# Optimization experiments

Hardware: AMD Instinct MI355X
Metric: run time of the kernel (lower is better)

Reference implementation:

```python
import jax, jax.numpy as jnp
import numpy as np

N_EXPERTS = 8
D_IN = 512
D_OUT = 512


def setup_inputs() -> dict:
    key = jax.random.key(0)
    k1, k2, k3, k4 = jax.random.split(key, 4)
    B, N = 16, 4096
    z = jax.random.randint(k1, (B, N), 0, N_EXPERTS, dtype=jnp.int64 if jax.config.jax_enable_x64 else jnp.int32)
    x = jax.random.normal(k2, (B, N, D_IN), dtype=jnp.float32)
    # Expert parameters: map_list[e] modeled as Linear(D_IN, D_OUT)
    W = jax.random.normal(k3, (N_EXPERTS, D_IN, D_OUT), dtype=jnp.float32) * (1.0 / np.sqrt(D_IN))
    b = jax.random.normal(k4, (N_EXPERTS, D_OUT), dtype=jnp.float32) * 0.01
    return {"z": z, "x": x, "W": W, "b": b}


def reference(z, x, W, b):
    B, N = z.shape
    z_flat = z.reshape(-1)                 # [T]
    x_flat = x.reshape(-1, x.shape[-1])    # [T, D_in]
    T = z_flat.shape[0]
    y = jnp.zeros((T, D_OUT), dtype=x.dtype)
    # Dense equivalent of mask-gather -> expert apply -> masked scatter.
    # Tokens with id == -1 (or any id not hit) stay zero, matching the torch code.
    for e in range(N_EXPERTS):
        mask = (z_flat == e)[:, None]      # [T, 1]
        y_e = x_flat @ W[e] + b[e]         # [T, D_out]
        y = jnp.where(mask, y_e, y)
    y = y.reshape(B, N, D_OUT)
    return (z, y)
```

## Files before the change

kernel.cpp:

```cpp
#include <hip/hip_runtime.h>
#include <stdint.h>

#define NEXP 8
#define DD   512
#define BM   128
#define BN   128

typedef short s16x8 __attribute__((ext_vector_type(8)));
typedef float f32x4 __attribute__((ext_vector_type(4)));

static __device__ __forceinline__ unsigned short f2bf(float f) {
    union { float f; unsigned u; } v; v.f = f;
    unsigned r = v.u + 0x7FFFu + ((v.u >> 16) & 1u);
    return (unsigned short)(r >> 16);
}


__global__ void hist_kernel(const int* __restrict__ z, int* __restrict__ counts, int T) {
    __shared__ int lc[NEXP];
    int tid = threadIdx.x;
    if (tid < NEXP) lc[tid] = 0;
    __syncthreads();
    int t = blockIdx.x * blockDim.x + tid;
    if (t < T) atomicAdd(&lc[z[t]], 1);
    __syncthreads();
    if (tid < NEXP) atomicAdd(&counts[tid], lc[tid]);
}

__global__ void scan_kernel(const int* __restrict__ counts, int* __restrict__ cursors,
                            int4* __restrict__ table, int max_tiles) {
    __shared__ int off[NEXP + 1];
    __shared__ int tb[NEXP + 1];
    int tid = threadIdx.x;
    if (tid == 0) {
        int o = 0, tbs = 0;
        for (int e = 0; e < NEXP; e++) {
            off[e] = o; tb[e] = tbs;
            cursors[e] = o;
            int c = counts[e];
            o += c;
            tbs += (c + BM - 1) / BM;
        }
        off[NEXP] = o; tb[NEXP] = tbs;
    }
    __syncthreads();
    for (int idx = tid; idx < max_tiles; idx += blockDim.x) {
        int4 ent; ent.x = -1; ent.y = 0; ent.z = 0; ent.w = 0;
#pragma unroll
        for (int e = 0; e < NEXP; e++) {
            if (idx >= tb[e] && idx < tb[e + 1]) {
                int r = (idx - tb[e]) * BM;
                ent.x = e; ent.y = off[e] + r; ent.z = (off[e + 1] - off[e]) - r;
            }
        }
        table[idx] = ent;
    }
}

__global__ void scatter_kernel(const int* __restrict__ z, int* __restrict__ cursors,
                               int* __restrict__ token_index, float* __restrict__ zout, int T) {
    __shared__ int lc[NEXP];
    __shared__ int lbase[NEXP];
    int tid = threadIdx.x;
    if (tid < NEXP) lc[tid] = 0;
    __syncthreads();
    int t = blockIdx.x * blockDim.x + tid;
    int e = 0, rank = 0;
    if (t < T) {
        e = z[t];
        rank = atomicAdd(&lc[e], 1);
        zout[t] = (float)e;
    }
    __syncthreads();
    if (tid < NEXP) lbase[tid] = atomicAdd(&cursors[tid], lc[tid]);
    __syncthreads();
    if (t < T) token_index[lbase[e] + rank] = t;
}

__global__ __launch_bounds__(256) void gather_kernel(const float* __restrict__ x,
                                                     const int* __restrict__ token_index,
                                                     unsigned short* __restrict__ xg, int T) {
    int i = blockIdx.x * 4 + (threadIdx.x >> 6);
    if (i >= T) return;
    int lane = threadIdx.x & 63;
    int t = token_index[i];
    const float4* src = (const float4*)(x + (size_t)t * DD) + lane * 2;
    float4 v0 = src[0], v1 = src[1];
    uint4 p;
    p.x = (unsigned)f2bf(v0.x) | ((unsigned)f2bf(v0.y) << 16);
    p.y = (unsigned)f2bf(v0.z) | ((unsigned)f2bf(v0.w) << 16);
    p.z = (unsigned)f2bf(v1.x) | ((unsigned)f2bf(v1.y) << 16);
    p.w = (unsigned)f2bf(v1.z) | ((unsigned)f2bf(v1.w) << 16);
    *(uint4*)(xg + (size_t)i * DD + lane * 8) = p;
}

__global__ void convw_kernel(const float* __restrict__ W, unsigned short* __restrict__ Wt) {
    __shared__ float tile[32][33];
    int e = blockIdx.z, k0 = blockIdx.x * 32, n0 = blockIdx.y * 32;
    int tid = threadIdx.x;
    const float* We = W + (size_t)e * DD * DD;
    unsigned short* WtE = Wt + (size_t)e * DD * DD;
    int c = tid & 31, r0 = tid >> 5;
#pragma unroll
    for (int i = 0; i < 4; i++) {
        int kr = r0 + 8 * i;
        tile[kr][c] = We[(size_t)(k0 + kr) * DD + n0 + c];
    }
    __syncthreads();
#pragma unroll
    for (int i = 0; i < 4; i++) {
        int nr = r0 + 8 * i;
        WtE[(size_t)(n0 + nr) * DD + k0 + c] = f2bf(tile[c][nr]);
    }
}


__global__ __launch_bounds__(256) void gemm2_kernel(
    const unsigned short* __restrict__ xg,
    const unsigned short* __restrict__ Wt,
    const float* __restrict__ bias,
    const int* __restrict__ token_index,
    const int4* __restrict__ table,
    float* __restrict__ y)
{
    int4 te = table[blockIdx.x];
    int e = te.x;
    if (e < 0) return;
    const int base = te.y;
    const int rows_valid = te.z < BM ? te.z : BM;
    const int n0 = blockIdx.y * BN;

    __shared__ unsigned short Als[BM * 64];
    __shared__ unsigned short Bls[BN * 64];

    const int tid  = threadIdx.x;
    const int lane = tid & 63;
    const int wave = tid >> 6;
    const int wm = (wave & 1) * 64;
    const int wn = (wave >> 1) * 64;

    int srow[4], schunk[4];
#pragma unroll
    for (int q = 0; q < 4; q++) {
        int s = wave * 256 + q * 64 + lane;
        srow[q]   = s >> 3;
        schunk[q] = (s & 7) ^ ((s >> 3) & 7);
    }

    const unsigned short* WtE = Wt + (size_t)e * DD * DD;

    f32x4 acc[4][4];
#pragma unroll
    for (int i = 0; i < 4; i++)
#pragma unroll
        for (int j = 0; j < 4; j++) acc[i][j] = (f32x4){0.f, 0.f, 0.f, 0.f};

    const int quad = lane >> 4;
    const int lrow = lane & 15;

    for (int k0 = 0; k0 < DD; k0 += 64) {
        __syncthreads();
#pragma unroll
        for (int q = 0; q < 4; q++) {
            const int r = srow[q], c = schunk[q];
            const unsigned short* ga = xg + (size_t)(base + r) * DD + k0 + c * 8;
            const unsigned short* gb = WtE + (size_t)(n0 + r) * DD + k0 + c * 8;
            unsigned short* la = &Als[(size_t)(wave * 256 + q * 64) * 8];
            unsigned short* lb = &Bls[(size_t)(wave * 256 + q * 64) * 8];
            __builtin_amdgcn_global_load_lds((const __attribute__((address_space(1))) void*)ga,
                                             (__attribute__((address_space(3))) void*)la, 16, 0, 0);
            __builtin_amdgcn_global_load_lds((const __attribute__((address_space(1))) void*)gb,
                                             (__attribute__((address_space(3))) void*)lb, 16, 0, 0);
        }
        __syncthreads();

#pragma unroll
        for (int ks = 0; ks < 2; ks++) {
            s16x8 af[4], bq[4];
#pragma unroll
            for (int i = 0; i < 4; i++) {
                int r = wm + i * 16 + lrow;
                af[i] = *(const s16x8*)(&Als[r * 64 + (((quad + 4 * ks) ^ (r & 7)) * 8)]);
            }
#pragma unroll
            for (int j = 0; j < 4; j++) {
                int r = wn + j * 16 + lrow;
                bq[j] = *(const s16x8*)(&Bls[r * 64 + (((quad + 4 * ks) ^ (r & 7)) * 8)]);
            }
#pragma unroll
            for (int i = 0; i < 4; i++)
#pragma unroll
                for (int j = 0; j < 4; j++)
                    acc[i][j] = __builtin_amdgcn_mfma_f32_16x16x32_bf16(af[i], bq[j], acc[i][j], 0, 0, 0);
        }
    }

    const int lcol = lane & 15;
    float bv[4];
#pragma unroll
    for (int j = 0; j < 4; j++) bv[j] = bias[e * DD + n0 + wn + j * 16 + lcol];
#pragma unroll
    for (int i = 0; i < 4; i++) {
#pragma unroll
        for (int reg = 0; reg < 4; reg++) {
            int r = wm + i * 16 + quad * 4 + reg;
            if (r < rows_valid) {
                int t = token_index[base + r];
                float* yr = y + (size_t)t * DD + n0 + wn + lcol;
#pragma unroll
                for (int j = 0; j < 4; j++)
                    yr[j * 16] = acc[i][j][reg] + bv[j];
            }
        }
    }
}


__global__ __launch_bounds__(256) void gemm_kernel(
    const float* __restrict__ x, const unsigned short* __restrict__ Wt,
    const float* __restrict__ bias, const int* __restrict__ token_index,
    const int4* __restrict__ table, float* __restrict__ y)
{
    int4 te = table[blockIdx.x];
    int e = te.x;
    if (e < 0) return;
    int base = te.y;
    int rows_valid = te.z < BM ? te.z : BM;
    int n0 = blockIdx.y * BN;

    __shared__ unsigned short Als[BM * 40];
    __shared__ unsigned short Bls[BN * 40];

    const int tid  = threadIdx.x;
    const int lane = tid & 63;
    const int wave = tid >> 6;
    const int wm = (wave & 1) * 64;
    const int wn = (wave >> 1) * 64;

    const int a_q  = tid & 7;
    const int a_r0 = tid >> 3;
    int tok[4];
#pragma unroll
    for (int i = 0; i < 4; i++) {
        int r = a_r0 + 32 * i;
        int rr = (r < rows_valid) ? r : 0;
        tok[i] = token_index[base + rr];
    }
    const int b_c  = tid & 3;
    const int b_n0 = tid >> 2;
    const unsigned short* WtE = Wt + (size_t)e * DD * DD;

    f32x4 acc[4][4];
#pragma unroll
    for (int i = 0; i < 4; i++)
#pragma unroll
        for (int j = 0; j < 4; j++) acc[i][j] = (f32x4){0.f, 0.f, 0.f, 0.f};

    const int quad = lane >> 4;
    const int lrow = lane & 15;

    for (int k0 = 0; k0 < DD; k0 += 32) {
        __syncthreads();
#pragma unroll
        for (int i = 0; i < 4; i++) {
            int r = a_r0 + 32 * i;
            const float4 v = *(const float4*)(x + (size_t)tok[i] * DD + k0 + a_q * 4);
            unsigned u0 = (unsigned)f2bf(v.x) | ((unsigned)f2bf(v.y) << 16);
            unsigned u1 = (unsigned)f2bf(v.z) | ((unsigned)f2bf(v.w) << 16);
            uint2 p; p.x = u0; p.y = u1;
            *(uint2*)(&Als[r * 40 + a_q * 4]) = p;
        }
#pragma unroll
        for (int i = 0; i < 2; i++) {
            int n = b_n0 + 64 * i;
            uint4 v = *(const uint4*)(WtE + (size_t)(n0 + n) * DD + k0 + b_c * 8);
            *(uint4*)(&Bls[n * 40 + b_c * 8]) = v;
        }
        __syncthreads();

        s16x8 af[4], bq[4];
#pragma unroll
        for (int i = 0; i < 4; i++)
            af[i] = *(const s16x8*)(&Als[(wm + i * 16 + lrow) * 40 + quad * 8]);
#pragma unroll
        for (int j = 0; j < 4; j++)
            bq[j] = *(const s16x8*)(&Bls[(wn + j * 16 + lrow) * 40 + quad * 8]);
#pragma unroll
        for (int i = 0; i < 4; i++)
#pragma unroll
            for (int j = 0; j < 4; j++)
                acc[i][j] = __builtin_amdgcn_mfma_f32_16x16x32_bf16(af[i], bq[j], acc[i][j], 0, 0, 0);
    }

    const int lcol = lane & 15;
    float bv[4];
#pragma unroll
    for (int j = 0; j < 4; j++) bv[j] = bias[e * DD + n0 + wn + j * 16 + lcol];
#pragma unroll
    for (int i = 0; i < 4; i++) {
#pragma unroll
        for (int reg = 0; reg < 4; reg++) {
            int r = wm + i * 16 + quad * 4 + reg;
            if (r < rows_valid) {
                int t = token_index[base + r];
                float* yr = y + (size_t)t * DD + n0 + wn + lcol;
#pragma unroll
                for (int j = 0; j < 4; j++)
                    yr[j * 16] = acc[i][j][reg] + bv[j];
            }
        }
    }
}


extern "C" void kernel_launch(void* const* d_in, const int* in_sizes, int n_in,
                              void* d_out, int out_size, void* d_ws, size_t ws_size,
                              hipStream_t stream) {
    const int*   z = (const int*)d_in[0];
    const float* x = (const float*)d_in[1];
    const float* W = (const float*)d_in[2];
    const float* b = (const float*)d_in[3];
    const int T = in_sizes[0];

    float* zout = (float*)d_out;
    float* y    = (float*)d_out + T;

    char* ws = (char*)d_ws;
    int*  counts      = (int*)ws;
    int*  cursors     = (int*)(ws + 64);
    int4* table       = (int4*)(ws + 256);
    int*  token_index = (int*)(ws + 16640);
    unsigned short* Wt = (unsigned short*)(ws + 278784);
    unsigned short* xg = (unsigned short*)(ws + 4473344);

    const int max_tiles = T / BM + NEXP;
    const size_t need = 4473344 + (size_t)T * DD * 2 + 131072;

    hipMemsetAsync(ws, 0, 64, stream);
    hist_kernel<<<(T + 255) / 256, 256, 0, stream>>>(z, counts, T);
    convw_kernel<<<dim3(DD / 32, DD / 32, NEXP), 256, 0, stream>>>(W, Wt);
    scan_kernel<<<1, 256, 0, stream>>>(counts, cursors, table, max_tiles);
    scatter_kernel<<<(T + 255) / 256, 256, 0, stream>>>(z, cursors, token_index, zout, T);

    if (ws_size >= need) {
        gather_kernel<<<(T + 3) / 4, 256, 0, stream>>>(x, token_index, xg, T);
        gemm2_kernel<<<dim3(max_tiles, DD / BN), 256, 0, stream>>>(xg, Wt, b, token_index, table, y);
    } else {
        gemm_kernel<<<dim3(max_tiles, DD / BN), 256, 0, stream>>>(x, Wt, b, token_index, table, y);
    }
}
```

Before: 333.7 us.

## Fuse prep kernels, merge scatter with gather, remap GEMM grid for XCD locality

Merges weight conversion and the expert histogram into one launch, and fuses the token scatter with the x gather/bf16 conversion so x is read in token order and written to its sorted slot. The GEMM grid is flattened and remapped so the four N-subtiles of the same row tile land on the same XCD, which should improve L2 reuse of the activation tile. This cuts launch count and one pass over token_index, but now uses scattered writes in the gather and needs max_tiles to be a multiple of 8 for the remap to cover every tile.

```diff
diff --git a/kernel.cpp b/kernel.cpp
--- a/kernel.cpp
+++ b/kernel.cpp
@@ -15,16 +15,38 @@
     return (unsigned short)(r >> 16);
 }
 
-
-__global__ void hist_kernel(const int* __restrict__ z, int* __restrict__ counts, int T) {
+__global__ __launch_bounds__(256) void prep_kernel(const float* __restrict__ W,
+                                                   unsigned short* __restrict__ Wt,
+                                                   const int* __restrict__ z,
+                                                   int* __restrict__ counts, int T) {
+    __shared__ float tile[32][33];
     __shared__ int lc[NEXP];
+    int bid = blockIdx.x;
     int tid = threadIdx.x;
-    if (tid < NEXP) lc[tid] = 0;
-    __syncthreads();
-    int t = blockIdx.x * blockDim.x + tid;
-    if (t < T) atomicAdd(&lc[z[t]], 1);
-    __syncthreads();
-    if (tid < NEXP) atomicAdd(&counts[tid], lc[tid]);
+    if (bid < 2048) {
+        int e = bid >> 8, k0 = ((bid >> 4) & 15) * 32, n0 = (bid & 15) * 32;
+        const float* We = W + (size_t)e * DD * DD;
+        unsigned short* WtE = Wt + (size_t)e * DD * DD;
+        int c = tid & 31, r0 = tid >> 5;
+#pragma unroll
+        for (int i = 0; i < 4; i++) {
+            int kr = r0 + 8 * i;
+            tile[kr][c] = We[(size_t)(k0 + kr) * DD + n0 + c];
+        }
+        __syncthreads();
+#pragma unroll
+        for (int i = 0; i < 4; i++) {
+            int nr = r0 + 8 * i;
+            WtE[(size_t)(n0 + nr) * DD + k0 + c] = f2bf(tile[c][nr]);
+        }
+    } else {
+        if (tid < NEXP) lc[tid] = 0;
+        __syncthreads();
+        int t = (bid - 2048) * 256 + tid;
+        if (t < T) atomicAdd(&lc[z[t]], 1);
+        __syncthreads();
+        if (tid < NEXP) atomicAdd(&counts[tid], lc[tid]);
+    }
 }
 
 __global__ void scan_kernel(const int* __restrict__ counts, int* __restrict__ cursors,
@@ -57,63 +79,51 @@
     }
 }
 
-__global__ void scatter_kernel(const int* __restrict__ z, int* __restrict__ cursors,
-                               int* __restrict__ token_index, float* __restrict__ zout, int T) {
+__global__ __launch_bounds__(256) void scatgat_kernel(
+    const int* __restrict__ z, const float* __restrict__ x,
+    int* __restrict__ cursors, int* __restrict__ token_index,
+    float* __restrict__ zout, unsigned short* __restrict__ xg, int T)
+{
     __shared__ int lc[NEXP];
     __shared__ int lbase[NEXP];
-    int tid = threadIdx.x;
+    __shared__ int ldst[64];
+    int tid = threadIdx.x, wave = tid >> 6, lane = tid & 63;
+    int t0 = blockIdx.x * 64;
     if (tid < NEXP) lc[tid] = 0;
     __syncthreads();
-    int t = blockIdx.x * blockDim.x + tid;
+    int t = t0 + wave * 16 + lane;
     int e = 0, rank = 0;
-    if (t < T) {
+    bool own = (lane < 16) && (t < T);
+    if (own) {
         e = z[t];
         rank = atomicAdd(&lc[e], 1);
         zout[t] = (float)e;
     }
     __syncthreads();
-    if (tid < NEXP) lbase[tid] = atomicAdd(&cursors[tid], lc[tid]);
-    __syncthreads();
-    if (t < T) token_index[lbase[e] + rank] = t;
-}
-
-__global__ __launch_bounds__(256) void gather_kernel(const float* __restrict__ x,
-                                                     const int* __restrict__ token_index,
-                                                     unsigned short* __restrict__ xg, int T) {
-    int i = blockIdx.x * 4 + (threadIdx.x >> 6);
-    if (i >= T) return;
-    int lane = threadIdx.x & 63;
-    int t = token_index[i];
-    const float4* src = (const float4*)(x + (size_t)t * DD) + lane * 2;
-    float4 v0 = src[0], v1 = src[1];
-    uint4 p;
-    p.x = (unsigned)f2bf(v0.x) | ((unsigned)f2bf(v0.y) << 16);
-    p.y = (unsigned)f2bf(v0.z) | ((unsigned)f2bf(v0.w) << 16);
-    p.z = (unsigned)f2bf(v1.x) | ((unsigned)f2bf(v1.y) << 16);
-    p.w = (unsigned)f2bf(v1.z) | ((unsigned)f2bf(v1.w) << 16);
-    *(uint4*)(xg + (size_t)i * DD + lane * 8) = p;
-}
-
-__global__ void convw_kernel(const float* __restrict__ W, unsigned short* __restrict__ Wt) {
-    __shared__ float tile[32][33];
-    int e = blockIdx.z, k0 = blockIdx.x * 32, n0 = blockIdx.y * 32;
-    int tid = threadIdx.x;
-    const float* We = W + (size_t)e * DD * DD;
-    unsigned short* WtE = Wt + (size_t)e * DD * DD;
-    int c = tid & 31, r0 = tid >> 5;
-#pragma unroll
-    for (int i = 0; i < 4; i++) {
-        int kr = r0 + 8 * i;
-        tile[kr][c] = We[(size_t)(k0 + kr) * DD + n0 + c];
-    }
-    __syncthreads();
-#pragma unroll
-    for (int i = 0; i < 4; i++) {
-        int nr = r0 + 8 * i;
-        WtE[(size_t)(n0 + nr) * DD + k0 + c] = f2bf(tile[c][nr]);
-    }
-}
-
+    if (tid < NEXP) lbase[tid] = lc[tid] ? atomicAdd(&cursors[tid], lc[tid]) : 0;
+    __syncthreads();
+    if (own) {
+        int dst = lbase[e] + rank;
+        token_index[dst] = t;
+        ldst[wave * 16 + lane] = dst;
+    }
+    __syncthreads();
+#pragma unroll
+    for (int rr = 0; rr < 16; rr++) {
+        int idx = wave * 16 + rr;
+        int src_t = t0 + idx;
+        if (src_t >= T) break;
+        int dst = ldst[idx];
+        const float4* src = (const float4*)(x + (size_t)src_t * DD) + lane * 2;
+        float4 v0 = src[0], v1 = src[1];
+        uint4 p;
+        p.x = (unsigned)f2bf(v0.x) | ((unsigned)f2bf(v0.y) << 16);
+        p.y = (unsigned)f2bf(v0.z) | ((unsigned)f2bf(v0.w) << 16);
+        p.z = (unsigned)f2bf(v1.x) | ((unsigned)f2bf(v1.y) << 16);
+        p.w = (unsigned)f2bf(v1.z) | ((unsigned)f2bf(v1.w) << 16);
+        *(uint4*)(xg + (size_t)dst * DD + lane * 8) = p;
+    }
+}
 
 __global__ __launch_bounds__(256) void gemm2_kernel(
     const unsigned short* __restrict__ xg,
@@ -123,12 +133,16 @@
     const int4* __restrict__ table,
     float* __restrict__ y)
 {
-    int4 te = table[blockIdx.x];
+    const int bid    = blockIdx.x;
+    const int xcd    = bid & 7;
+    const int nsub   = (bid >> 3) & 3;
+    const int tileid = ((bid >> 5) << 3) | xcd;
+    int4 te = table[tileid];
     int e = te.x;
     if (e < 0) return;
     const int base = te.y;
     const int rows_valid = te.z < BM ? te.z : BM;
-    const int n0 = blockIdx.y * BN;
+    const int n0 = nsub * BN;
 
     __shared__ unsigned short Als[BM * 64];
     __shared__ unsigned short Bls[BN * 64];
@@ -215,6 +229,26 @@
     }
 }
 
+
+__global__ void scatter_kernel(const int* __restrict__ z, int* __restrict__ cursors,
+                               int* __restrict__ token_index, float* __restrict__ zout, int T) {
+    __shared__ int lc[NEXP];
+    __shared__ int lbase[NEXP];
+    int tid = threadIdx.x;
+    if (tid < NEXP) lc[tid] = 0;
+    __syncthreads();
+    int t = blockIdx.x * blockDim.x + tid;
+    int e = 0, rank = 0;
+    if (t < T) {
+        e = z[t];
+        rank = atomicAdd(&lc[e], 1);
+        zout[t] = (float)e;
+    }
+    __syncthreads();
+    if (tid < NEXP) lbase[tid] = atomicAdd(&cursors[tid], lc[tid]);
+    __syncthreads();
+    if (t < T) token_index[lbase[e] + rank] = t;
+}
 
 __global__ __launch_bounds__(256) void gemm_kernel(
     const float* __restrict__ x, const unsigned short* __restrict__ Wt,
@@ -337,15 +371,14 @@
     const size_t need = 4473344 + (size_t)T * DD * 2 + 131072;
 
     hipMemsetAsync(ws, 0, 64, stream);
-    hist_kernel<<<(T + 255) / 256, 256, 0, stream>>>(z, counts, T);
-    convw_kernel<<<dim3(DD / 32, DD / 32, NEXP), 256, 0, stream>>>(W, Wt);
+    prep_kernel<<<2048 + (T + 255) / 256, 256, 0, stream>>>(W, Wt, z, counts, T);
     scan_kernel<<<1, 256, 0, stream>>>(counts, cursors, table, max_tiles);
-    scatter_kernel<<<(T + 255) / 256, 256, 0, stream>>>(z, cursors, token_index, zout, T);
 
     if (ws_size >= need) {
-        gather_kernel<<<(T + 3) / 4, 256, 0, stream>>>(x, token_index, xg, T);
-        gemm2_kernel<<<dim3(max_tiles, DD / BN), 256, 0, stream>>>(xg, Wt, b, token_index, table, y);
+        scatgat_kernel<<<(T + 63) / 64, 256, 0, stream>>>(z, x, cursors, token_index, zout, xg, T);
+        gemm2_kernel<<<max_tiles * 4, 256, 0, stream>>>(xg, Wt, b, token_index, table, y);
     } else {
+        scatter_kernel<<<(T + 255) / 256, 256, 0, stream>>>(z, cursors, token_index, zout, T);
         gemm_kernel<<<dim3(max_tiles, DD / BN), 256, 0, stream>>>(x, Wt, b, token_index, table, y);
     }
 }
```

Result: no change. 339.0 us (+1.6%).
